# Kernel optimization log

Measured on AMD Instinct MI355X. Metric: run time of the kernel, lower is better.

Reference implementation:

```python
import jax, jax.numpy as jnp
import numpy as np

N = 100000   # nodes
E = 1200000  # edges
D = 64       # feature dim (in_channels == out_channels)


def gcn_layer(x, W, src, dst):
    # GCNConv(normalize=False, bias=False, aggr='add'):
    # linear transform then scatter-add of source messages into targets.
    h = x @ W                                            # [N, D]
    msg = h[src]                                         # [E, D] gather
    return jax.ops.segment_sum(msg, dst, num_segments=x.shape[0])  # [N, D]


def setup_inputs() -> dict:
    key = jax.random.key(0)
    ks = jax.random.split(key, 5)
    x = jax.random.normal(ks[0], (N, D), dtype=jnp.float32)
    edge_index = jax.random.randint(ks[1], (2, E), 0, N, dtype=jnp.int64)
    scale = 1.0 / np.sqrt(D).astype(np.float32)
    W0 = jax.random.normal(ks[2], (D, D), dtype=jnp.float32) * scale
    W1 = jax.random.normal(ks[3], (D, D), dtype=jnp.float32) * scale
    W2 = jax.random.normal(ks[4], (D, D), dtype=jnp.float32) * scale
    return {"x": x, "edge_index": edge_index, "W0": W0, "W1": W1, "W2": W2}


def reference(x, edge_index, W0, W1, W2):
    src = edge_index[0]  # messages flow source -> target (PyG default)
    dst = edge_index[1]
    # num_hop = 3 stacked convs; dropout p=0 and use_bn=False are no-ops.
    for W in (W0, W1, W2):
        x = gcn_layer(x, W, src, dst)
    return x
```

## Files before the change

### kernel.cpp

```cpp
#include <hip/hip_runtime.h>


#define GCN_D 64
#define SEGSHIFT 8
#define SEGROWS 256
#define MAXSEG 512
#define A_EPB 4096

typedef unsigned short ushort;

__device__ __forceinline__ float bf2f(ushort u) {
    union { unsigned u; float f; } c; c.u = ((unsigned)u) << 16; return c.f;
}
__device__ __forceinline__ ushort f2bf(float f) {
    union { float f; unsigned u; } c; c.f = f;
    const unsigned r = 0x7FFFu + ((c.u >> 16) & 1u);
    return (ushort)((c.u + r) >> 16);
}

__global__ __launch_bounds__(256) void k_wchain(const float* __restrict__ W0,
                                                const float* __restrict__ W1,
                                                const float* __restrict__ W2,
                                                float* __restrict__ Wc,
                                                int* __restrict__ ghist) {
    __shared__ float A[4096], B[4096], T[4096];
    const int t = threadIdx.x;
    for (int i = t; i < MAXSEG; i += 256) ghist[i] = 0;
    for (int i = t; i < 1024; i += 256) {
        ((float4*)A)[i] = ((const float4*)W0)[i];
        ((float4*)B)[i] = ((const float4*)W1)[i];
    }
    __syncthreads();
#pragma unroll
    for (int g = 0; g < 4; ++g) {
        const int idx = t + 256 * g;
        const int r = idx >> 4, c4 = idx & 15;
        float4 acc = make_float4(0.f, 0.f, 0.f, 0.f);
#pragma unroll
        for (int k = 0; k < 64; ++k) {
            const float a = A[r * 64 + k];
            const float4 b = ((float4*)B)[k * 16 + c4];
            acc.x = fmaf(a, b.x, acc.x); acc.y = fmaf(a, b.y, acc.y);
            acc.z = fmaf(a, b.z, acc.z); acc.w = fmaf(a, b.w, acc.w);
        }
        ((float4*)T)[idx] = acc;
    }
    __syncthreads();
    for (int i = t; i < 1024; i += 256) ((float4*)B)[i] = ((const float4*)W2)[i];
    __syncthreads();
#pragma unroll
    for (int g = 0; g < 4; ++g) {
        const int idx = t + 256 * g;
        const int r = idx >> 4, c4 = idx & 15;
        float4 acc = make_float4(0.f, 0.f, 0.f, 0.f);
#pragma unroll
        for (int k = 0; k < 64; ++k) {
            const float a = T[r * 64 + k];
            const float4 b = ((float4*)B)[k * 16 + c4];
            acc.x = fmaf(a, b.x, acc.x); acc.y = fmaf(a, b.y, acc.y);
            acc.z = fmaf(a, b.z, acc.z); acc.w = fmaf(a, b.w, acc.w);
        }
        ((float4*)Wc)[idx] = acc;
    }
}

__global__ __launch_bounds__(256) void k_gemmcvt(const float* __restrict__ X,
                                                 const float* __restrict__ Wc,
                                                 ushort* __restrict__ B,
                                                 int nrows) {
    __shared__ float Wl[64 * 64];
    __shared__ float Xl[16][65];
    const int tid = threadIdx.x;
    for (int i = tid; i < 1024; i += 256) ((float4*)Wl)[i] = ((const float4*)Wc)[i];

    const int lr = tid >> 4;
    const int lc = tid & 15;
    const int grow = blockIdx.x * 16 + lr;

    if (grow < nrows) {
        const float4 xv = ((const float4*)X)[(size_t)grow * 16 + lc];
        Xl[lr][lc * 4 + 0] = xv.x; Xl[lr][lc * 4 + 1] = xv.y;
        Xl[lr][lc * 4 + 2] = xv.z; Xl[lr][lc * 4 + 3] = xv.w;
    }
    __syncthreads();

    float4 acc = make_float4(0.f, 0.f, 0.f, 0.f);
#pragma unroll
    for (int k = 0; k < 64; ++k) {
        const float xv = Xl[lr][k];
        const float4 w4 = ((const float4*)Wl)[k * 16 + lc];
        acc.x = fmaf(xv, w4.x, acc.x); acc.y = fmaf(xv, w4.y, acc.y);
        acc.z = fmaf(xv, w4.z, acc.z); acc.w = fmaf(xv, w4.w, acc.w);
    }
    if (grow < nrows) {
        ushort4 o;
        o.x = f2bf(acc.x); o.y = f2bf(acc.y); o.z = f2bf(acc.z); o.w = f2bf(acc.w);
        ((ushort4*)B)[(size_t)grow * 16 + lc] = o;
    }
}

__global__ __launch_bounds__(256) void k_a0(const int* __restrict__ ei,
                                            int* __restrict__ ghist, int E) {
    __shared__ int h[MAXSEG];
    const int t = threadIdx.x;
    for (int i = t; i < MAXSEG; i += 256) h[i] = 0;
    __syncthreads();
    for (int e = blockIdx.x * 256 + t; e < E; e += gridDim.x * 256)
        atomicAdd(&h[ei[E + e] >> SEGSHIFT], 1);
    __syncthreads();
    for (int i = t; i < MAXSEG; i += 256) {
        const int c = h[i];
        if (c) atomicAdd(&ghist[i], c);
    }
}

__global__ __launch_bounds__(MAXSEG) void k_ascan(const int* __restrict__ ghist,
                                                  int* __restrict__ gOff,
                                                  int* __restrict__ gcur,
                                                  int* __restrict__ rp, int N, int E) {
    __shared__ int sd[MAXSEG];
    const int t = threadIdx.x;
    const int v = ghist[t];
    sd[t] = v; __syncthreads();
    for (int off = 1; off < MAXSEG; off <<= 1) {
        const int y = (t >= off) ? sd[t - off] : 0;
        __syncthreads();
        sd[t] += y;
        __syncthreads();
    }
    const int excl = sd[t] - v;
    gOff[t] = excl; gcur[t] = excl;
    if (t == MAXSEG - 1) gOff[MAXSEG] = sd[t];
    if (t == 0) rp[N] = E;
}

__global__ __launch_bounds__(512) void k_apart(const int* __restrict__ ei,
                                               int* __restrict__ gcur,
                                               unsigned* __restrict__ ebuf, int E) {
    __shared__ int hist[MAXSEG], lofs[MAXSEG], cur[MAXSEG], gbase[MAXSEG];
    __shared__ unsigned stg[A_EPB];
    __shared__ ushort stg2[A_EPB];
    const int t = threadIdx.x;
    const int base = blockIdx.x * A_EPB;
    const int cnt = min(A_EPB, E - base);

    hist[t] = 0;
    __syncthreads();

    unsigned my[8]; int mb[8];
#pragma unroll
    for (int j = 0; j < 8; ++j) {
        const int i = t + j * 512;
        if (i < cnt) {
            const int e = base + i;
            const unsigned s = (unsigned)ei[e];
            const unsigned d = (unsigned)ei[E + e];
            my[j] = (s << 8) | (d & (SEGROWS - 1));
            mb[j] = (int)(d >> SEGSHIFT);
            atomicAdd(&hist[mb[j]], 1);
        } else mb[j] = -1;
    }
    __syncthreads();

    {
        const int v = hist[t];
        lofs[t] = v; __syncthreads();
        for (int off = 1; off < MAXSEG; off <<= 1) {
            const int y = (t >= off) ? lofs[t - off] : 0;
            __syncthreads();
            lofs[t] += y;
            __syncthreads();
        }
        const int excl = lofs[t] - v;
        __syncthreads();
        lofs[t] = excl; cur[t] = excl;
    }
    __syncthreads();

#pragma unroll
    for (int j = 0; j < 8; ++j) {
        if (mb[j] >= 0) {
            const int p = atomicAdd(&cur[mb[j]], 1);
            stg[p] = my[j];
            stg2[p] = (ushort)mb[j];
        }
    }
    __syncthreads();

    {
        const int c = hist[t];
        gbase[t] = c ? atomicAdd(&gcur[t], c) : 0;
    }
    __syncthreads();

    for (int i = t; i < cnt; i += 512) {
        const int b = (int)stg2[i];
        ebuf[(size_t)gbase[b] + (unsigned)(i - lofs[b])] = stg[i];
    }
}

__global__ __launch_bounds__(SEGROWS) void k_bplace(const unsigned* __restrict__ ebuf,
                                                    const int* __restrict__ gOff,
                                                    int* __restrict__ rp,
                                                    int* __restrict__ cs, int N) {
    __shared__ int h[SEGROWS], ofs[SEGROWS];
    const int s = blockIdx.x;
    const int t = threadIdx.x;
    const int e0 = gOff[s];
    const int e1 = gOff[s + 1];

    h[t] = 0; __syncthreads();
    for (int e = e0 + t; e < e1; e += SEGROWS)
        atomicAdd(&h[ebuf[e] & (SEGROWS - 1)], 1);
    __syncthreads();

    const int v = h[t];
    ofs[t] = v; __syncthreads();
    for (int off = 1; off < SEGROWS; off <<= 1) {
        const int y = (t >= off) ? ofs[t - off] : 0;
        __syncthreads();
        ofs[t] += y;
        __syncthreads();
    }
    const int excl = ofs[t] - v;
    const int r = s * SEGROWS + t;
    if (r < N) rp[r] = e0 + excl;
    __syncthreads();
    ofs[t] = excl;
    __syncthreads();

    for (int e = e0 + t; e < e1; e += SEGROWS) {
        const unsigned pr = ebuf[e];
        const int lr = (int)(pr & (SEGROWS - 1));
        const int p = atomicAdd(&ofs[lr], 1);
        cs[e0 + p] = (int)(pr >> 8);
    }
}

__global__ __launch_bounds__(256) void k_aggc(const ushort* __restrict__ B,
                                              const int* __restrict__ rp,
                                              const int* __restrict__ cs,
                                              ushort* __restrict__ out, int N) {
    const int t = threadIdx.x;
    const int gw = (blockIdx.x * 256 + t) >> 6;
    const int lane = t & 63;
    const int f4 = lane & 15;
    const int r = gw * 4 + (lane >> 4);
    if (r >= N) return;

    const int e0 = rp[r];
    const int e1 = rp[r + 1];
    const ushort4* Bv = (const ushort4*)B;

    float4 acc = make_float4(0.f, 0.f, 0.f, 0.f);
    int e = e0;
    for (; e + 7 < e1; e += 8) {
        ushort4 u[8];
#pragma unroll
        for (int j = 0; j < 8; ++j) u[j] = Bv[(size_t)cs[e + j] * 16 + f4];
#pragma unroll
        for (int j = 0; j < 8; ++j) {
            acc.x += bf2f(u[j].x); acc.y += bf2f(u[j].y);
            acc.z += bf2f(u[j].z); acc.w += bf2f(u[j].w);
        }
    }
    for (; e + 3 < e1; e += 4) {
        ushort4 u[4];
#pragma unroll
        for (int j = 0; j < 4; ++j) u[j] = Bv[(size_t)cs[e + j] * 16 + f4];
#pragma unroll
        for (int j = 0; j < 4; ++j) {
            acc.x += bf2f(u[j].x); acc.y += bf2f(u[j].y);
            acc.z += bf2f(u[j].z); acc.w += bf2f(u[j].w);
        }
    }
    for (; e < e1; ++e) {
        const ushort4 u = Bv[(size_t)cs[e] * 16 + f4];
        acc.x += bf2f(u.x); acc.y += bf2f(u.y);
        acc.z += bf2f(u.z); acc.w += bf2f(u.w);
    }
    ushort4 o;
    o.x = f2bf(acc.x); o.y = f2bf(acc.y); o.z = f2bf(acc.z); o.w = f2bf(acc.w);
    ((ushort4*)out)[(size_t)r * 16 + f4] = o;
}

__global__ __launch_bounds__(256) void k_aggw(const ushort* __restrict__ B,
                                              const int* __restrict__ rp,
                                              const int* __restrict__ cs,
                                              float* __restrict__ out, int N) {
    const int t = threadIdx.x;
    const int gw = (blockIdx.x * 256 + t) >> 6;
    const int lane = t & 63;
    const int f4 = lane & 15;
    const int r = gw * 4 + (lane >> 4);
    if (r >= N) return;

    const int e0 = rp[r];
    const int e1 = rp[r + 1];
    const ushort4* Bv = (const ushort4*)B;

    float4 acc = make_float4(0.f, 0.f, 0.f, 0.f);
    int e = e0;
    for (; e + 7 < e1; e += 8) {
        ushort4 u[8];
#pragma unroll
        for (int j = 0; j < 8; ++j) u[j] = Bv[(size_t)cs[e + j] * 16 + f4];
#pragma unroll
        for (int j = 0; j < 8; ++j) {
            acc.x += bf2f(u[j].x); acc.y += bf2f(u[j].y);
            acc.z += bf2f(u[j].z); acc.w += bf2f(u[j].w);
        }
    }
    for (; e + 3 < e1; e += 4) {
        ushort4 u[4];
#pragma unroll
        for (int j = 0; j < 4; ++j) u[j] = Bv[(size_t)cs[e + j] * 16 + f4];
#pragma unroll
        for (int j = 0; j < 4; ++j) {
            acc.x += bf2f(u[j].x); acc.y += bf2f(u[j].y);
            acc.z += bf2f(u[j].z); acc.w += bf2f(u[j].w);
        }
    }
    for (; e < e1; ++e) {
        const ushort4 u = Bv[(size_t)cs[e] * 16 + f4];
        acc.x += bf2f(u.x); acc.y += bf2f(u.y);
        acc.z += bf2f(u.z); acc.w += bf2f(u.w);
    }
    ((float4*)out)[(size_t)r * 16 + f4] = acc;
}

__global__ __launch_bounds__(256) void gcn_gemm64(const float* __restrict__ X,
                                                  const float* __restrict__ W,
                                                  float* __restrict__ H,
                                                  int nrows) {
    __shared__ float Wl[64 * 64];
    __shared__ float Xl[16][65];
    const int tid = threadIdx.x;
    for (int i = tid; i < 1024; i += 256) ((float4*)Wl)[i] = ((const float4*)W)[i];
    const int rowBase = blockIdx.x * 16;
    const int lr = tid >> 4;
    const int lc = tid & 15;
    const int grow = rowBase + lr;
    if (grow < nrows) {
        float4 xv = ((const float4*)X)[(long long)grow * 16 + lc];
        Xl[lr][lc * 4 + 0] = xv.x; Xl[lr][lc * 4 + 1] = xv.y;
        Xl[lr][lc * 4 + 2] = xv.z; Xl[lr][lc * 4 + 3] = xv.w;
    }
    __syncthreads();
    float4 acc = make_float4(0.f, 0.f, 0.f, 0.f);
#pragma unroll
    for (int k = 0; k < 64; ++k) {
        const float xv = Xl[lr][k];
        const float4 w4 = ((float4*)Wl)[k * 16 + lc];
        acc.x = fmaf(xv, w4.x, acc.x); acc.y = fmaf(xv, w4.y, acc.y);
        acc.z = fmaf(xv, w4.z, acc.z); acc.w = fmaf(xv, w4.w, acc.w);
    }
    if (grow < nrows) ((float4*)H)[(long long)grow * 16 + lc] = acc;
}

__global__ __launch_bounds__(256) void gcn_scatter(const float* __restrict__ H,
                                                   const int* __restrict__ ei,
                                                   float* __restrict__ out,
                                                   int nedges) {
    const long long t = (long long)blockIdx.x * 256 + threadIdx.x;
    const int e = (int)(t >> 4);
    if (e >= nedges) return;
    const int lc = (int)(t & 15);
    const int s = ei[e];
    const int d = ei[nedges + e];
    const float4 v = ((const float4*)H)[(long long)s * 16 + lc];
    float* o = out + (long long)d * GCN_D + lc * 4;
    atomicAdd(o + 0, v.x);
    atomicAdd(o + 1, v.y);
    atomicAdd(o + 2, v.z);
    atomicAdd(o + 3, v.w);
}

extern "C" void kernel_launch(void* const* d_in, const int* in_sizes, int n_in,
                              void* d_out, int out_size, void* d_ws, size_t ws_size,
                              hipStream_t stream) {
    const float* x  = (const float*)d_in[0];
    const int*   ei = (const int*)d_in[1];
    const float* W0 = (const float*)d_in[2];
    const float* W1 = (const float*)d_in[3];
    const float* W2 = (const float*)d_in[4];
    float* out = (float*)d_out;

    const int N_ = in_sizes[0] / GCN_D;
    const int E_ = in_sizes[1] / 2;
    const int NSEG = (N_ + SEGROWS - 1) >> SEGSHIFT;

    uintptr_t base = (uintptr_t)d_ws;
    ushort* B0 = (ushort*)base;
    const size_t bfBytes  = (size_t)N_ * GCN_D * 2;
    const size_t regBytes = bfBytes > (size_t)E_ * 4 ? bfBytes : (size_t)E_ * 4;
    ushort*   B1   = (ushort*)(base + bfBytes);
    unsigned* ebuf = (unsigned*)B1;
    int* rp    = (int*)(base + bfBytes + regBytes);
    int* gOff  = rp + (N_ + 2);
    int* ghist = gOff + (MAXSEG + 1);
    int* gcur  = ghist + MAXSEG;
    float* Wc  = (float*)(gcur + MAXSEG);
    int* cs    = (int*)(Wc + 4096);
    const size_t needed = ((uintptr_t)(cs + E_) - base);

    const int gemmBlocks = (N_ + 15) / 16;

    if (NSEG <= MAXSEG && N_ < (1 << 24) && ws_size >= needed) {
        k_wchain<<<1, 256, 0, stream>>>(W0, W1, W2, Wc, ghist);
        k_gemmcvt<<<gemmBlocks, 256, 0, stream>>>(x, Wc, B0, N_);
        k_a0<<<512, 256, 0, stream>>>(ei, ghist, E_);
        k_ascan<<<1, MAXSEG, 0, stream>>>(ghist, gOff, gcur, rp, N_, E_);
        k_apart<<<(E_ + A_EPB - 1) / A_EPB, 512, 0, stream>>>(ei, gcur, ebuf, E_);
        k_bplace<<<NSEG, SEGROWS, 0, stream>>>(ebuf, gOff, rp, cs, N_);

        const int aggBlocks = (N_ + 15) / 16;
        k_aggc<<<aggBlocks, 256, 0, stream>>>(B0, rp, cs, B1, N_);
        k_aggc<<<aggBlocks, 256, 0, stream>>>(B1, rp, cs, B0, N_);
        k_aggw<<<aggBlocks, 256, 0, stream>>>(B0, rp, cs, out, N_);
    } else {
        float* h = (float*)d_ws;
        const int scatBlocks = (int)(((long long)E_ * 16 + 255) / 256);
        const float* curAct = x;
        for (int l = 0; l < 3; ++l) {
            const float* Wl = (l == 0) ? W0 : (l == 1) ? W1 : W2;
            gcn_gemm64<<<gemmBlocks, 256, 0, stream>>>(curAct, Wl, h, N_);
            hipMemsetAsync(out, 0, (size_t)N_ * GCN_D * sizeof(float), stream);
            gcn_scatter<<<scatBlocks, 256, 0, stream>>>(h, ei, out, E_);
            curAct = out;
        }
    }
}
```

Before: 172.4 us.

## Fuse histogram into GEMM, fold scans into partition kernels, add 8-lane aggregation

Moves the destination-segment histogram into the GEMM/convert kernel and drops the standalone histogram and scan kernels. The partition and placement kernels now recompute the segment prefix sum from the global histogram in every block, which removes two launches at the cost of redundant per-block scans. A new first-layer aggregation kernel gives each row 8 lanes with 16-byte loads and an 8-way unrolled gather to increase memory-level parallelism. The other two layers keep the original aggregation kernels.

```diff
diff --git a/kernel.cpp b/kernel.cpp
--- a/kernel.cpp
+++ b/kernel.cpp
@@ -6,26 +6,37 @@
 #define SEGROWS 256
 #define MAXSEG 512
 #define A_EPB 4096
+#define HISTB 512
 
 typedef unsigned short ushort;
 
 __device__ __forceinline__ float bf2f(ushort u) {
     union { unsigned u; float f; } c; c.u = ((unsigned)u) << 16; return c.f;
+}
+__device__ __forceinline__ float bflo(unsigned u) {
+    union { unsigned u; float f; } c; c.u = u << 16; return c.f;
+}
+__device__ __forceinline__ float bfhi(unsigned u) {
+    union { unsigned u; float f; } c; c.u = u & 0xFFFF0000u; return c.f;
 }
 __device__ __forceinline__ ushort f2bf(float f) {
     union { float f; unsigned u; } c; c.f = f;
     const unsigned r = 0x7FFFu + ((c.u >> 16) & 1u);
     return (ushort)((c.u + r) >> 16);
 }
+__device__ __forceinline__ unsigned pack2(float a, float b) {
+    return (unsigned)f2bf(a) | ((unsigned)f2bf(b) << 16);
+}
 
 __global__ __launch_bounds__(256) void k_wchain(const float* __restrict__ W0,
                                                 const float* __restrict__ W1,
                                                 const float* __restrict__ W2,
                                                 float* __restrict__ Wc,
-                                                int* __restrict__ ghist) {
+                                                int* __restrict__ ghist,
+                                                int* __restrict__ csr0) {
     __shared__ float A[4096], B[4096], T[4096];
     const int t = threadIdx.x;
-    for (int i = t; i < MAXSEG; i += 256) ghist[i] = 0;
+    for (int i = t; i < MAXSEG; i += 256) { ghist[i] = 0; csr0[i] = 0; }
     for (int i = t; i < 1024; i += 256) {
         ((float4*)A)[i] = ((const float4*)W0)[i];
         ((float4*)B)[i] = ((const float4*)W1)[i];
@@ -67,9 +78,12 @@
 __global__ __launch_bounds__(256) void k_gemmcvt(const float* __restrict__ X,
                                                  const float* __restrict__ Wc,
                                                  ushort* __restrict__ B,
-                                                 int nrows) {
-    __shared__ float Wl[64 * 64];
+                                                 const int* __restrict__ ei,
+                                                 int* __restrict__ ghist,
+                                                 int nrows, int E) {
+    __shared__ float Wl[4096];
     __shared__ float Xl[16][65];
+    __shared__ int h[MAXSEG];
     const int tid = threadIdx.x;
     for (int i = tid; i < 1024; i += 256) ((float4*)Wl)[i] = ((const float4*)Wc)[i];
 
@@ -97,53 +111,41 @@
         o.x = f2bf(acc.x); o.y = f2bf(acc.y); o.z = f2bf(acc.z); o.w = f2bf(acc.w);
         ((ushort4*)B)[(size_t)grow * 16 + lc] = o;
     }
-}
-
-__global__ __launch_bounds__(256) void k_a0(const int* __restrict__ ei,
-                                            int* __restrict__ ghist, int E) {
-    __shared__ int h[MAXSEG];
-    const int t = threadIdx.x;
-    for (int i = t; i < MAXSEG; i += 256) h[i] = 0;
-    __syncthreads();
-    for (int e = blockIdx.x * 256 + t; e < E; e += gridDim.x * 256)
-        atomicAdd(&h[ei[E + e] >> SEGSHIFT], 1);
-    __syncthreads();
-    for (int i = t; i < MAXSEG; i += 256) {
-        const int c = h[i];
-        if (c) atomicAdd(&ghist[i], c);
-    }
-}
-
-__global__ __launch_bounds__(MAXSEG) void k_ascan(const int* __restrict__ ghist,
-                                                  int* __restrict__ gOff,
-                                                  int* __restrict__ gcur,
-                                                  int* __restrict__ rp, int N, int E) {
-    __shared__ int sd[MAXSEG];
-    const int t = threadIdx.x;
-    const int v = ghist[t];
-    sd[t] = v; __syncthreads();
-    for (int off = 1; off < MAXSEG; off <<= 1) {
-        const int y = (t >= off) ? sd[t - off] : 0;
-        __syncthreads();
-        sd[t] += y;
-        __syncthreads();
-    }
-    const int excl = sd[t] - v;
-    gOff[t] = excl; gcur[t] = excl;
-    if (t == MAXSEG - 1) gOff[MAXSEG] = sd[t];
-    if (t == 0) rp[N] = E;
+
+    if (blockIdx.x < HISTB) {
+        for (int i = tid; i < MAXSEG; i += 256) h[i] = 0;
+        __syncthreads();
+        for (int e = blockIdx.x * 256 + tid; e < E; e += HISTB * 256)
+            atomicAdd(&h[ei[E + e] >> SEGSHIFT], 1);
+        __syncthreads();
+        for (int i = tid; i < MAXSEG; i += 256) {
+            const int c = h[i];
+            if (c) atomicAdd(&ghist[i], c);
+        }
+    }
 }
 
 __global__ __launch_bounds__(512) void k_apart(const int* __restrict__ ei,
-                                               int* __restrict__ gcur,
+                                               const int* __restrict__ ghist,
+                                               int* __restrict__ csr0,
                                                unsigned* __restrict__ ebuf, int E) {
-    __shared__ int hist[MAXSEG], lofs[MAXSEG], cur[MAXSEG], gbase[MAXSEG];
+    __shared__ int hist[MAXSEG], lofs[MAXSEG], cur[MAXSEG], gbase[MAXSEG], goffx[MAXSEG];
     __shared__ unsigned stg[A_EPB];
     __shared__ ushort stg2[A_EPB];
     const int t = threadIdx.x;
     const int base = blockIdx.x * A_EPB;
     const int cnt = min(A_EPB, E - base);
 
+    const int gv = ghist[t];
+    goffx[t] = gv; __syncthreads();
+    for (int off = 1; off < MAXSEG; off <<= 1) {
+        const int y = (t >= off) ? goffx[t - off] : 0;
+        __syncthreads();
+        goffx[t] += y;
+        __syncthreads();
+    }
+    const int gexcl = goffx[t] - gv;
+    goffx[t] = gexcl;
     hist[t] = 0;
     __syncthreads();
 
@@ -189,7 +191,8 @@
 
     {
         const int c = hist[t];
-        gbase[t] = c ? atomicAdd(&gcur[t], c) : 0;
+        const int p = c ? atomicAdd(&csr0[t], c) : 0;
+        gbase[t] = goffx[t] + p;
     }
     __syncthreads();
 
@@ -200,14 +203,32 @@
 }
 
 __global__ __launch_bounds__(SEGROWS) void k_bplace(const unsigned* __restrict__ ebuf,
-                                                    const int* __restrict__ gOff,
+                                                    const int* __restrict__ ghist,
                                                     int* __restrict__ rp,
-                                                    int* __restrict__ cs, int N) {
-    __shared__ int h[SEGROWS], ofs[SEGROWS];
+                                                    int* __restrict__ cs, int N, int E) {
+    __shared__ int h[SEGROWS], ofs[SEGROWS], gpart[SEGROWS];
+    __shared__ int gx[MAXSEG];
     const int s = blockIdx.x;
     const int t = threadIdx.x;
-    const int e0 = gOff[s];
-    const int e1 = gOff[s + 1];
+
+    const int a0 = ghist[2 * t];
+    const int a1 = ghist[2 * t + 1];
+    const int ps = a0 + a1;
+    gpart[t] = ps; __syncthreads();
+    for (int off = 1; off < SEGROWS; off <<= 1) {
+        const int y = (t >= off) ? gpart[t - off] : 0;
+        __syncthreads();
+        gpart[t] += y;
+        __syncthreads();
+    }
+    const int ex = gpart[t] - ps;
+    gx[2 * t] = ex;
+    gx[2 * t + 1] = ex + a0;
+    if (s == 0 && t == 0) rp[N] = E;
+    __syncthreads();
+
+    const int e0 = gx[s];
+    const int e1 = e0 + ghist[s];
 
     h[t] = 0; __syncthreads();
     for (int e = e0 + t; e < e1; e += SEGROWS)
@@ -235,6 +256,48 @@
         const int p = atomicAdd(&ofs[lr], 1);
         cs[e0 + p] = (int)(pr >> 8);
     }
+}
+
+__global__ __launch_bounds__(256) void k_aggc2(const ushort* __restrict__ B,
+                                               const int* __restrict__ rp,
+                                               const int* __restrict__ cs,
+                                               ushort* __restrict__ out, int N) {
+    const int t = threadIdx.x;
+    const int gw = (blockIdx.x * 256 + t) >> 6;
+    const int lane = t & 63;
+    const int f8 = lane & 7;
+    const int r = gw * 8 + (lane >> 3);
+    if (r >= N) return;
+
+    const int e0 = rp[r];
+    const int e1 = rp[r + 1];
+    const uint4* Bv = (const uint4*)B;
+
+    float acc[8] = {0.f, 0.f, 0.f, 0.f, 0.f, 0.f, 0.f, 0.f};
+    int e = e0;
+    for (; e + 7 < e1; e += 8) {
+        uint4 u[8];
+#pragma unroll
+        for (int j = 0; j < 8; ++j) u[j] = Bv[(size_t)cs[e + j] * 8 + f8];
+#pragma unroll
+        for (int j = 0; j < 8; ++j) {
+            acc[0] += bflo(u[j].x); acc[1] += bfhi(u[j].x);
+            acc[2] += bflo(u[j].y); acc[3] += bfhi(u[j].y);
+            acc[4] += bflo(u[j].z); acc[5] += bfhi(u[j].z);
+            acc[6] += bflo(u[j].w); acc[7] += bfhi(u[j].w);
+        }
+    }
+    for (; e < e1; ++e) {
+        const uint4 u = Bv[(size_t)cs[e] * 8 + f8];
+        acc[0] += bflo(u.x); acc[1] += bfhi(u.x);
+        acc[2] += bflo(u.y); acc[3] += bfhi(u.y);
+        acc[4] += bflo(u.z); acc[5] += bfhi(u.z);
+        acc[6] += bflo(u.w); acc[7] += bfhi(u.w);
+    }
+    uint4 o;
+    o.x = pack2(acc[0], acc[1]); o.y = pack2(acc[2], acc[3]);
+    o.z = pack2(acc[4], acc[5]); o.w = pack2(acc[6], acc[7]);
+    ((uint4*)out)[(size_t)r * 8 + f8] = o;
 }
 
 __global__ __launch_bounds__(256) void k_aggc(const ushort* __restrict__ B,
@@ -397,27 +460,26 @@
     ushort*   B1   = (ushort*)(base + bfBytes);
     unsigned* ebuf = (unsigned*)B1;
     int* rp    = (int*)(base + bfBytes + regBytes);
-    int* gOff  = rp + (N_ + 2);
-    int* ghist = gOff + (MAXSEG + 1);
-    int* gcur  = ghist + MAXSEG;
-    float* Wc  = (float*)(gcur + MAXSEG);
+    int* ghist = rp + (N_ + 2);
+    int* csr0  = ghist + MAXSEG;
+    float* Wc  = (float*)(csr0 + MAXSEG);
     int* cs    = (int*)(Wc + 4096);
     const size_t needed = ((uintptr_t)(cs + E_) - base);
 
     const int gemmBlocks = (N_ + 15) / 16;
+    const int gcBlocks = gemmBlocks > HISTB ? gemmBlocks : HISTB;
 
     if (NSEG <= MAXSEG && N_ < (1 << 24) && ws_size >= needed) {
-        k_wchain<<<1, 256, 0, stream>>>(W0, W1, W2, Wc, ghist);
-        k_gemmcvt<<<gemmBlocks, 256, 0, stream>>>(x, Wc, B0, N_);
-        k_a0<<<512, 256, 0, stream>>>(ei, ghist, E_);
-        k_ascan<<<1, MAXSEG, 0, stream>>>(ghist, gOff, gcur, rp, N_, E_);
-        k_apart<<<(E_ + A_EPB - 1) / A_EPB, 512, 0, stream>>>(ei, gcur, ebuf, E_);
-        k_bplace<<<NSEG, SEGROWS, 0, stream>>>(ebuf, gOff, rp, cs, N_);
-
-        const int aggBlocks = (N_ + 15) / 16;
-        k_aggc<<<aggBlocks, 256, 0, stream>>>(B0, rp, cs, B1, N_);
-        k_aggc<<<aggBlocks, 256, 0, stream>>>(B1, rp, cs, B0, N_);
-        k_aggw<<<aggBlocks, 256, 0, stream>>>(B0, rp, cs, out, N_);
+        k_wchain<<<1, 256, 0, stream>>>(W0, W1, W2, Wc, ghist, csr0);
+        k_gemmcvt<<<gcBlocks, 256, 0, stream>>>(x, Wc, B0, ei, ghist, N_, E_);
+        k_apart<<<(E_ + A_EPB - 1) / A_EPB, 512, 0, stream>>>(ei, ghist, csr0, ebuf, E_);
+        k_bplace<<<NSEG, SEGROWS, 0, stream>>>(ebuf, ghist, rp, cs, N_, E_);
+
+        const int aggBlocks  = (N_ + 15) / 16;
+        const int aggBlocks2 = (N_ + 31) / 32;
+        k_aggc2<<<aggBlocks2, 256, 0, stream>>>(B0, rp, cs, B1, N_);
+        k_aggc <<<aggBlocks,  256, 0, stream>>>(B1, rp, cs, B0, N_);
+        k_aggw <<<aggBlocks,  256, 0, stream>>>(B0, rp, cs, out, N_);
     } else {
         float* h = (float*)d_ws;
         const int scatBlocks = (int)(((long long)E_ * 16 + 255) / 256);
```

Measured after the change: 169.4 us. No clear change (-1.7%).
